# Optimization experiments

Measured on AMD Instinct MI355X. Metric: run time of the kernel, lower is better.

Reference implementation:

```python
import jax, jax.numpy as jnp
import numpy as np

EPS = 1e-12
SHRINK = 0.0025

def _l2norm(x, axis=1):
    return x / jnp.maximum(jnp.linalg.norm(x, axis=axis, keepdims=True), EPS)

def setup_inputs() -> dict:
    key = jax.random.key(0)
    ks = jax.random.split(key, 6)
    N, C, H, W = 32, 512, 32, 32
    mem_dim, spatial = 512, H * W
    hid = spatial // 2
    x = jax.random.normal(ks[0], (N, C, H, W), dtype=jnp.float32)
    memory = jax.random.normal(ks[1], (mem_dim, spatial), dtype=jnp.float32)
    memory = _l2norm(memory, axis=1)  # buffer is L2-normalized at init
    w1 = jax.random.normal(ks[2], (hid, spatial), dtype=jnp.float32) * 0.02
    b1 = jax.random.normal(ks[3], (hid,), dtype=jnp.float32) * 0.02
    w2 = jax.random.normal(ks[4], (spatial, hid), dtype=jnp.float32) * 0.02
    b2 = jax.random.normal(ks[5], (spatial,), dtype=jnp.float32) * 0.02
    return {"x": x, "memory": memory, "w1": w1, "b1": b1, "w2": w2, "b2": b2}

def reference(x, memory, w1, b1, w2, b2):
    N, C, H, W = x.shape
    mem_dim = memory.shape[0]
    input_flat = x.reshape(N * C, H * W)
    input_norm = _l2norm(input_flat, axis=1)
    # shared MLP over memory bank: Linear -> ReLU -> Linear -> ReLU
    h = jax.nn.relu(memory @ w1.T + b1)
    mem_proc = jax.nn.relu(h @ w2.T + b2)
    memory_norm = _l2norm(mem_proc, axis=1)
    # addressing: cosine sim -> softmax -> hard shrink -> L1 renorm
    att = jax.nn.softmax(input_norm @ memory_norm.T, axis=1)  # [N*C, M]
    att = jax.nn.relu(att - SHRINK)
    att = att / jnp.maximum(att.sum(axis=1, keepdims=True), EPS)  # p=1 norm (att >= 0)
    output = (att @ memory_norm).reshape(N, C, H, W)
    att_channel_avg = att.reshape(N, C, mem_dim).mean(axis=1)  # [N, M]
    att_spatial = jnp.broadcast_to(att_channel_avg[:, :, None, None], (N, mem_dim, H, W))
    return output, att_spatial, input_flat, memory_norm, att
```

## Files before the change

kernel.cpp:

```cpp
#include <hip/hip_runtime.h>

typedef float  f32x4  __attribute__((ext_vector_type(4)));
typedef __bf16 bf16x8 __attribute__((ext_vector_type(8)));
typedef __bf16 bf16x4 __attribute__((ext_vector_type(4)));

#define L2EPS   1e-12f
#define SHRINKC 0.0025f


__device__ __forceinline__ bf16x8 pack_bf16(f32x4 v0, f32x4 v1) {
  bf16x8 r;
  r[0] = (__bf16)v0[0]; r[1] = (__bf16)v0[1]; r[2] = (__bf16)v0[2]; r[3] = (__bf16)v0[3];
  r[4] = (__bf16)v1[0]; r[5] = (__bf16)v1[1]; r[6] = (__bf16)v1[2]; r[7] = (__bf16)v1[3];
  return r;
}

__device__ __forceinline__ bf16x8 load_cvt_bf16x8(const float* p) {
  const f32x4* q = (const f32x4*)p;
  return pack_bf16(q[0], q[1]);
}

__device__ __forceinline__ float dot4(f32x4 v) {
  return v[0]*v[0] + v[1]*v[1] + v[2]*v[2] + v[3]*v[3];
}

__global__ __launch_bounds__(64) void gemm1(
    const float* __restrict__ A, const float* __restrict__ B,
    const float* __restrict__ bias, float* __restrict__ C,
    float* __restrict__ attsum) {
  const int bid = blockIdx.y * gridDim.x + blockIdx.x;
  attsum[bid * 64 + threadIdx.x] = 0.f;

  const int K = 1024, N = 512;
  const int r0   = blockIdx.x * 32;
  const int n0   = blockIdx.y * 32;
  const int lane = threadIdx.x & 63;
  const int quad = lane >> 4;
  const int m    = lane & 15;

  f32x4 acc[2][2] = {};
  for (int k0 = 0; k0 < K; k0 += 32) {
    const int kk = k0 + quad * 8;
    bf16x8 a[2], b[2];
    #pragma unroll
    for (int rg = 0; rg < 2; ++rg)
      a[rg] = load_cvt_bf16x8(A + (size_t)(r0 + rg * 16 + m) * K + kk);
    #pragma unroll
    for (int cf = 0; cf < 2; ++cf)
      b[cf] = load_cvt_bf16x8(B + (size_t)(n0 + cf * 16 + m) * K + kk);
    #pragma unroll
    for (int rg = 0; rg < 2; ++rg)
      #pragma unroll
      for (int cf = 0; cf < 2; ++cf)
        acc[rg][cf] = __builtin_amdgcn_mfma_f32_16x16x32_bf16(a[rg], b[cf], acc[rg][cf], 0, 0, 0);
  }
  #pragma unroll
  for (int rg = 0; rg < 2; ++rg)
    #pragma unroll
    for (int cf = 0; cf < 2; ++cf) {
      const int n = n0 + cf * 16 + m;
      const float bv = bias[n];
      #pragma unroll
      for (int vi = 0; vi < 4; ++vi) {
        const int r = r0 + rg * 16 + quad * 4 + vi;
        C[(size_t)r * N + n] = fmaxf(acc[rg][cf][vi] + bv, 0.f);
      }
    }
}

__global__ __launch_bounds__(64) void gemm2(
    const float* __restrict__ A, const float* __restrict__ B,
    const float* __restrict__ bias, float* __restrict__ C) {
  const int K = 512, N = 1024;
  const int r0   = blockIdx.x * 32;
  const int n0   = blockIdx.y * 32;
  const int lane = threadIdx.x & 63;
  const int quad = lane >> 4;
  const int m    = lane & 15;

  f32x4 acc[2][2] = {};
  for (int k0 = 0; k0 < K; k0 += 32) {
    const int kk = k0 + quad * 8;
    bf16x8 a[2], b[2];
    #pragma unroll
    for (int rg = 0; rg < 2; ++rg)
      a[rg] = load_cvt_bf16x8(A + (size_t)(r0 + rg * 16 + m) * K + kk);
    #pragma unroll
    for (int cf = 0; cf < 2; ++cf)
      b[cf] = load_cvt_bf16x8(B + (size_t)(n0 + cf * 16 + m) * K + kk);
    #pragma unroll
    for (int rg = 0; rg < 2; ++rg)
      #pragma unroll
      for (int cf = 0; cf < 2; ++cf)
        acc[rg][cf] = __builtin_amdgcn_mfma_f32_16x16x32_bf16(a[rg], b[cf], acc[rg][cf], 0, 0, 0);
  }
  #pragma unroll
  for (int rg = 0; rg < 2; ++rg)
    #pragma unroll
    for (int cf = 0; cf < 2; ++cf) {
      const int n = n0 + cf * 16 + m;
      const float bv = bias[n];
      #pragma unroll
      for (int vi = 0; vi < 4; ++vi) {
        const int r = r0 + rg * 16 + quad * 4 + vi;
        C[(size_t)r * N + n] = fmaxf(acc[rg][cf][vi] + bv, 0.f);
      }
    }
}

__global__ __launch_bounds__(256) void norm_rows(
    const float* __restrict__ mp, float* __restrict__ mn_f32,
    __bf16* __restrict__ mn_bf16) {
  const int r = blockIdx.x;
  const int tid = threadIdx.x;
  const f32x4 v = *(const f32x4*)(mp + (size_t)r * 1024 + tid * 4);
  float ss = dot4(v);
  #pragma unroll
  for (int d = 1; d < 64; d <<= 1) ss += __shfl_xor(ss, d);
  __shared__ float wsum[4];
  __shared__ float invs;
  if ((tid & 63) == 0) wsum[tid >> 6] = ss;
  __syncthreads();
  if (tid == 0) {
    float t = wsum[0] + wsum[1] + wsum[2] + wsum[3];
    invs = 1.f / fmaxf(sqrtf(t), L2EPS);
  }
  __syncthreads();
  const float iv = invs;
  f32x4 o = v * iv;
  *(f32x4*)(mn_f32 + (size_t)r * 1024 + tid * 4) = o;
  bf16x4 ob;
  ob[0] = (__bf16)o[0]; ob[1] = (__bf16)o[1]; ob[2] = (__bf16)o[2]; ob[3] = (__bf16)o[3];
  *(bf16x4*)(mn_bf16 + (size_t)r * 1024 + tid * 4) = ob;
}

__global__ __launch_bounds__(256) void attend(
    const float* __restrict__ x, const __bf16* __restrict__ Mn,
    const float* __restrict__ Mnf, float* __restrict__ out_flat,
    float* __restrict__ out_out, float* __restrict__ out_att,
    float* __restrict__ attsum) {
  __shared__ float S[32][512];
  __shared__ float invn[32];
  const int r0   = blockIdx.x * 32;
  const int tid  = threadIdx.x;
  const int wave = tid >> 6;
  const int lane = tid & 63;
  const int quad = lane >> 4;
  const int m    = lane & 15;
  const int n0w  = wave * 128;

  float ss0 = 0.f, ss1 = 0.f;
  f32x4 acc[8][2] = {};
  for (int k0 = 0; k0 < 1024; k0 += 32) {
    const int kk = k0 + quad * 8;
    bf16x8 a[2];
    f32x4 v0a, v0b, v1a, v1b;
    {
      const int row = r0 + m;
      const f32x4* q = (const f32x4*)(x + (size_t)row * 1024 + kk);
      v0a = q[0]; v0b = q[1];
      a[0] = pack_bf16(v0a, v0b);
      ss0 += dot4(v0a) + dot4(v0b);
    }
    {
      const int row = r0 + 16 + m;
      const f32x4* q = (const f32x4*)(x + (size_t)row * 1024 + kk);
      v1a = q[0]; v1b = q[1];
      a[1] = pack_bf16(v1a, v1b);
      ss1 += dot4(v1a) + dot4(v1b);
    }
    if (wave == 0) {
      float* d0 = out_flat + (size_t)(r0 + m) * 1024 + kk;
      float* d1 = out_flat + (size_t)(r0 + 16 + m) * 1024 + kk;
      *(f32x4*)d0 = v0a; *(f32x4*)(d0 + 4) = v0b;
      *(f32x4*)d1 = v1a; *(f32x4*)(d1 + 4) = v1b;
    }
    #pragma unroll
    for (int nf = 0; nf < 8; ++nf) {
      const bf16x8 b = *(const bf16x8*)(Mn + (size_t)(n0w + nf * 16 + m) * 1024 + kk);
      acc[nf][0] = __builtin_amdgcn_mfma_f32_16x16x32_bf16(a[0], b, acc[nf][0], 0, 0, 0);
      acc[nf][1] = __builtin_amdgcn_mfma_f32_16x16x32_bf16(a[1], b, acc[nf][1], 0, 0, 0);
    }
  }
  ss0 += __shfl_xor(ss0, 16); ss0 += __shfl_xor(ss0, 32);
  ss1 += __shfl_xor(ss1, 16); ss1 += __shfl_xor(ss1, 32);
  if (wave == 0 && quad == 0) {
    invn[m]      = 1.f / fmaxf(sqrtf(ss0), L2EPS);
    invn[16 + m] = 1.f / fmaxf(sqrtf(ss1), L2EPS);
  }
  #pragma unroll
  for (int nf = 0; nf < 8; ++nf)
    #pragma unroll
    for (int rg = 0; rg < 2; ++rg)
      #pragma unroll
      for (int vi = 0; vi < 4; ++vi)
        S[rg * 16 + quad * 4 + vi][n0w + nf * 16 + m] = acc[nf][rg][vi];
  __syncthreads();

  const int row = tid >> 3;
  const int sub = tid & 7;
  const float iv = invn[row];
  float se = 0.f;
  for (int i = 0; i < 64; ++i) {
    const int c = (sub + 4 * row + 8 * i) & 511;
    const float e = __expf(S[row][c] * iv);
    S[row][c] = e;
    se += e;
  }
  #pragma unroll
  for (int d = 1; d < 8; d <<= 1) se += __shfl_xor(se, d);
  const float inv_se = 1.f / se;
  float rsum = 0.f;
  for (int i = 0; i < 64; ++i) {
    const int c = (sub + 4 * row + 8 * i) & 511;
    const float sh = fmaxf(S[row][c] * inv_se - SHRINKC, 0.f);
    S[row][c] = sh;
    rsum += sh;
  }
  #pragma unroll
  for (int d = 1; d < 8; d <<= 1) rsum += __shfl_xor(rsum, d);
  const float invr = 1.f / fmaxf(rsum, L2EPS);
  for (int i = 0; i < 64; ++i) {
    const int c = (sub + 4 * row + 8 * i) & 511;
    S[row][c] *= invr;
  }
  const int any = __syncthreads_or((sub == 0) && (rsum > 0.f));

  {
    float* dst = out_att + (size_t)r0 * 512;
    for (int idx = tid; idx < 32 * 512 / 4; idx += 256) {
      const int f = idx * 4;
      *(f32x4*)(dst + f) = *(const f32x4*)(&S[f >> 9][f & 511]);
    }
  }

  if (!any) {
    const f32x4 z = {0.f, 0.f, 0.f, 0.f};
    float* dst = out_out + (size_t)r0 * 1024;
    for (int idx = tid; idx < 32 * 1024 / 4; idx += 256)
      *(f32x4*)(dst + idx * 4) = z;
  } else {
    const int nimg = r0 >> 9;
    for (int c = tid; c < 512; c += 256) {
      float s = 0.f;
      for (int rr = 0; rr < 32; ++rr) s += S[rr][c];
      atomicAdd(&attsum[nimg * 512 + c], s);
    }
    const int c0 = tid * 4;
    for (int rr = 0; rr < 32; ++rr) {
      f32x4 o = {0.f, 0.f, 0.f, 0.f};
      for (int mm = 0; mm < 512; ++mm) {
        const float a = S[rr][mm];
        o += a * (*(const f32x4*)(Mnf + (size_t)mm * 1024 + c0));
      }
      *(f32x4*)(out_out + (size_t)(r0 + rr) * 1024 + c0) = o;
    }
  }
}

__global__ __launch_bounds__(256) void spread(
    const float* __restrict__ attsum, float* __restrict__ out_sp) {
  const int nm = blockIdx.x;
  const float v = attsum[nm] * (1.f / 512.f);
  const f32x4 vv = {v, v, v, v};
  *(f32x4*)(out_sp + (size_t)nm * 1024 + threadIdx.x * 4) = vv;
}


extern "C" void kernel_launch(void* const* d_in, const int* in_sizes, int n_in,
                              void* d_out, int out_size, void* d_ws, size_t ws_size,
                              hipStream_t stream) {
  const float* x      = (const float*)d_in[0];
  const float* memory = (const float*)d_in[1];
  const float* w1     = (const float*)d_in[2];
  const float* b1     = (const float*)d_in[3];
  const float* w2     = (const float*)d_in[4];
  const float* b2     = (const float*)d_in[5];

  float* out = (float*)d_out;
  float* out_output = out;
  float* out_attsp  = out + 16777216;
  float* out_flat   = out + 33554432;
  float* out_mnorm  = out + 50331648;
  float* out_att    = out + 50855936;

  char* ws = (char*)d_ws;
  float*  h      = (float*)ws;
  float*  mp     = (float*)(ws + (1 << 20));
  __bf16* mnb    = (__bf16*)(ws + (1 << 20) + (2 << 20));
  float*  attsum = (float*)(ws + (1 << 20) + (2 << 20) + (1 << 20));

  gemm1<<<dim3(16, 16), 64, 0, stream>>>(memory, w1, b1, h, attsum);
  gemm2<<<dim3(16, 32), 64, 0, stream>>>(h, w2, b2, mp);
  norm_rows<<<512, 256, 0, stream>>>(mp, out_mnorm, mnb);
  attend<<<512, 256, 0, stream>>>(x, mnb, out_mnorm, out_flat, out_output, out_att, attsum);
  spread<<<16384, 256, 0, stream>>>(attsum, out_attsp);
}
```

Before: 414.2 us.

## Keep softmax in MFMA registers, drop LDS score tile, coarsen spread kernel

The MFMA operands are swapped so the accumulator layout puts the 32 input rows along lanes. Softmax, hard shrink and L1 renormalisation then run directly on the accumulator registers, with cross-wave row reductions through a small LDS buffer. This removes the 64KB LDS score tile, which raises occupancy and cuts LDS traffic. The att@Mn GEMV now re-reads attention rows from global memory (out_att) instead of LDS, so correctness relies on block-level visibility of those writes, and it adds global read traffic. Each spread block also writes 8 rows, reducing the launch to fewer blocks.

```diff
diff --git a/kernel.cpp b/kernel.cpp
--- a/kernel.cpp
+++ b/kernel.cpp
@@ -139,8 +139,7 @@
     const float* __restrict__ Mnf, float* __restrict__ out_flat,
     float* __restrict__ out_out, float* __restrict__ out_att,
     float* __restrict__ attsum) {
-  __shared__ float S[32][512];
-  __shared__ float invn[32];
+  __shared__ float red[2][4][32];
   const int r0   = blockIdx.x * 32;
   const int tid  = threadIdx.x;
   const int wave = tid >> 6;
@@ -153,20 +152,18 @@
   f32x4 acc[8][2] = {};
   for (int k0 = 0; k0 < 1024; k0 += 32) {
     const int kk = k0 + quad * 8;
-    bf16x8 a[2];
+    bf16x8 b[2];
     f32x4 v0a, v0b, v1a, v1b;
     {
-      const int row = r0 + m;
-      const f32x4* q = (const f32x4*)(x + (size_t)row * 1024 + kk);
+      const f32x4* q = (const f32x4*)(x + (size_t)(r0 + m) * 1024 + kk);
       v0a = q[0]; v0b = q[1];
-      a[0] = pack_bf16(v0a, v0b);
+      b[0] = pack_bf16(v0a, v0b);
       ss0 += dot4(v0a) + dot4(v0b);
     }
     {
-      const int row = r0 + 16 + m;
-      const f32x4* q = (const f32x4*)(x + (size_t)row * 1024 + kk);
+      const f32x4* q = (const f32x4*)(x + (size_t)(r0 + 16 + m) * 1024 + kk);
       v1a = q[0]; v1b = q[1];
-      a[1] = pack_bf16(v1a, v1b);
+      b[1] = pack_bf16(v1a, v1b);
       ss1 += dot4(v1a) + dot4(v1b);
     }
     if (wave == 0) {
@@ -177,62 +174,63 @@
     }
     #pragma unroll
     for (int nf = 0; nf < 8; ++nf) {
-      const bf16x8 b = *(const bf16x8*)(Mn + (size_t)(n0w + nf * 16 + m) * 1024 + kk);
-      acc[nf][0] = __builtin_amdgcn_mfma_f32_16x16x32_bf16(a[0], b, acc[nf][0], 0, 0, 0);
-      acc[nf][1] = __builtin_amdgcn_mfma_f32_16x16x32_bf16(a[1], b, acc[nf][1], 0, 0, 0);
+      const bf16x8 a = *(const bf16x8*)(Mn + (size_t)(n0w + nf * 16 + m) * 1024 + kk);
+      acc[nf][0] = __builtin_amdgcn_mfma_f32_16x16x32_bf16(a, b[0], acc[nf][0], 0, 0, 0);
+      acc[nf][1] = __builtin_amdgcn_mfma_f32_16x16x32_bf16(a, b[1], acc[nf][1], 0, 0, 0);
     }
   }
   ss0 += __shfl_xor(ss0, 16); ss0 += __shfl_xor(ss0, 32);
   ss1 += __shfl_xor(ss1, 16); ss1 += __shfl_xor(ss1, 32);
-  if (wave == 0 && quad == 0) {
-    invn[m]      = 1.f / fmaxf(sqrtf(ss0), L2EPS);
-    invn[16 + m] = 1.f / fmaxf(sqrtf(ss1), L2EPS);
-  }
+  const float iv0 = 1.f / fmaxf(sqrtf(ss0), L2EPS);
+  const float iv1 = 1.f / fmaxf(sqrtf(ss1), L2EPS);
+
+  float se0 = 0.f, se1 = 0.f;
   #pragma unroll
   for (int nf = 0; nf < 8; ++nf)
     #pragma unroll
-    for (int rg = 0; rg < 2; ++rg)
-      #pragma unroll
-      for (int vi = 0; vi < 4; ++vi)
-        S[rg * 16 + quad * 4 + vi][n0w + nf * 16 + m] = acc[nf][rg][vi];
+    for (int vi = 0; vi < 4; ++vi) {
+      const float e0 = __expf(acc[nf][0][vi] * iv0);
+      const float e1 = __expf(acc[nf][1][vi] * iv1);
+      acc[nf][0][vi] = e0; acc[nf][1][vi] = e1;
+      se0 += e0; se1 += e1;
+    }
+  se0 += __shfl_xor(se0, 16); se0 += __shfl_xor(se0, 32);
+  se1 += __shfl_xor(se1, 16); se1 += __shfl_xor(se1, 32);
+  if (quad == 0) { red[0][wave][m] = se0; red[0][wave][16 + m] = se1; }
   __syncthreads();
-
-  const int row = tid >> 3;
-  const int sub = tid & 7;
-  const float iv = invn[row];
-  float se = 0.f;
-  for (int i = 0; i < 64; ++i) {
-    const int c = (sub + 4 * row + 8 * i) & 511;
-    const float e = __expf(S[row][c] * iv);
-    S[row][c] = e;
-    se += e;
-  }
-  #pragma unroll
-  for (int d = 1; d < 8; d <<= 1) se += __shfl_xor(se, d);
-  const float inv_se = 1.f / se;
-  float rsum = 0.f;
-  for (int i = 0; i < 64; ++i) {
-    const int c = (sub + 4 * row + 8 * i) & 511;
-    const float sh = fmaxf(S[row][c] * inv_se - SHRINKC, 0.f);
-    S[row][c] = sh;
-    rsum += sh;
-  }
-  #pragma unroll
-  for (int d = 1; d < 8; d <<= 1) rsum += __shfl_xor(rsum, d);
-  const float invr = 1.f / fmaxf(rsum, L2EPS);
-  for (int i = 0; i < 64; ++i) {
-    const int c = (sub + 4 * row + 8 * i) & 511;
-    S[row][c] *= invr;
-  }
-  const int any = __syncthreads_or((sub == 0) && (rsum > 0.f));
-
-  {
-    float* dst = out_att + (size_t)r0 * 512;
-    for (int idx = tid; idx < 32 * 512 / 4; idx += 256) {
-      const int f = idx * 4;
-      *(f32x4*)(dst + f) = *(const f32x4*)(&S[f >> 9][f & 511]);
-    }
-  }
+  const float te0 = red[0][0][m] + red[0][1][m] + red[0][2][m] + red[0][3][m];
+  const float te1 = red[0][0][16 + m] + red[0][1][16 + m] + red[0][2][16 + m] + red[0][3][16 + m];
+  const float ie0 = 1.f / te0;
+  const float ie1 = 1.f / te1;
+
+  float rs0 = 0.f, rs1 = 0.f;
+  #pragma unroll
+  for (int nf = 0; nf < 8; ++nf)
+    #pragma unroll
+    for (int vi = 0; vi < 4; ++vi) {
+      const float s0 = fmaxf(acc[nf][0][vi] * ie0 - SHRINKC, 0.f);
+      const float s1 = fmaxf(acc[nf][1][vi] * ie1 - SHRINKC, 0.f);
+      acc[nf][0][vi] = s0; acc[nf][1][vi] = s1;
+      rs0 += s0; rs1 += s1;
+    }
+  rs0 += __shfl_xor(rs0, 16); rs0 += __shfl_xor(rs0, 32);
+  rs1 += __shfl_xor(rs1, 16); rs1 += __shfl_xor(rs1, 32);
+  if (quad == 0) { red[1][wave][m] = rs0; red[1][wave][16 + m] = rs1; }
+  __syncthreads();
+  const float tr0 = red[1][0][m] + red[1][1][m] + red[1][2][m] + red[1][3][m];
+  const float tr1 = red[1][0][16 + m] + red[1][1][16 + m] + red[1][2][16 + m] + red[1][3][16 + m];
+  const float ir0 = 1.f / fmaxf(tr0, L2EPS);
+  const float ir1 = 1.f / fmaxf(tr1, L2EPS);
+
+  #pragma unroll
+  for (int nf = 0; nf < 8; ++nf) {
+    acc[nf][0] *= ir0;
+    acc[nf][1] *= ir1;
+    *(f32x4*)(out_att + (size_t)(r0 + m)      * 512 + n0w + nf * 16 + quad * 4) = acc[nf][0];
+    *(f32x4*)(out_att + (size_t)(r0 + 16 + m) * 512 + n0w + nf * 16 + quad * 4) = acc[nf][1];
+  }
+  __threadfence_block();
+  const int any = __syncthreads_or(tr0 + tr1 > 0.f);
 
   if (!any) {
     const f32x4 z = {0.f, 0.f, 0.f, 0.f};
@@ -241,16 +239,28 @@
       *(f32x4*)(dst + idx * 4) = z;
   } else {
     const int nimg = r0 >> 9;
-    for (int c = tid; c < 512; c += 256) {
-      float s = 0.f;
-      for (int rr = 0; rr < 32; ++rr) s += S[rr][c];
-      atomicAdd(&attsum[nimg * 512 + c], s);
+    #pragma unroll
+    for (int nf = 0; nf < 8; ++nf) {
+      f32x4 v = acc[nf][0] + acc[nf][1];
+      #pragma unroll
+      for (int d = 1; d < 16; d <<= 1) {
+        v[0] += __shfl_xor(v[0], d); v[1] += __shfl_xor(v[1], d);
+        v[2] += __shfl_xor(v[2], d); v[3] += __shfl_xor(v[3], d);
+      }
+      if (m == 0) {
+        const int c = n0w + nf * 16 + quad * 4;
+        atomicAdd(&attsum[nimg * 512 + c + 0], v[0]);
+        atomicAdd(&attsum[nimg * 512 + c + 1], v[1]);
+        atomicAdd(&attsum[nimg * 512 + c + 2], v[2]);
+        atomicAdd(&attsum[nimg * 512 + c + 3], v[3]);
+      }
     }
     const int c0 = tid * 4;
     for (int rr = 0; rr < 32; ++rr) {
+      const float* arow = out_att + (size_t)(r0 + rr) * 512;
       f32x4 o = {0.f, 0.f, 0.f, 0.f};
       for (int mm = 0; mm < 512; ++mm) {
-        const float a = S[rr][mm];
+        const float a = arow[mm];
         o += a * (*(const f32x4*)(Mnf + (size_t)mm * 1024 + c0));
       }
       *(f32x4*)(out_out + (size_t)(r0 + rr) * 1024 + c0) = o;
@@ -260,10 +270,14 @@
 
 __global__ __launch_bounds__(256) void spread(
     const float* __restrict__ attsum, float* __restrict__ out_sp) {
-  const int nm = blockIdx.x;
-  const float v = attsum[nm] * (1.f / 512.f);
-  const f32x4 vv = {v, v, v, v};
-  *(f32x4*)(out_sp + (size_t)nm * 1024 + threadIdx.x * 4) = vv;
+  const int base = blockIdx.x * 8;
+  #pragma unroll
+  for (int p = 0; p < 8; ++p) {
+    const int nm = base + p;
+    const float v = attsum[nm] * (1.f / 512.f);
+    const f32x4 vv = {v, v, v, v};
+    *(f32x4*)(out_sp + (size_t)nm * 1024 + threadIdx.x * 4) = vv;
+  }
 }
 
 
@@ -294,5 +308,5 @@
   gemm2<<<dim3(16, 32), 64, 0, stream>>>(h, w2, b2, mp);
   norm_rows<<<512, 256, 0, stream>>>(mp, out_mnorm, mnb);
   attend<<<512, 256, 0, stream>>>(x, mnb, out_mnorm, out_flat, out_output, out_att, attsum);
-  spread<<<16384, 256, 0, stream>>>(attsum, out_attsp);
-}
+  spread<<<2048, 256, 0, stream>>>(attsum, out_attsp);
+}
```

Result: no change. 410.8 us (-0.8%).
